# Performance work log

Measured on AMD Instinct MI355X. Metric: run time of the kernel, lower is better.

## Reference

```python
import jax, jax.numpy as jnp
import numpy as np

LMAX_IN = 3
LMAX_OUT = 3
C = 64          # num_channel
H = 64          # num_channel_hidden
N_NODES = 2048
N_EDGES = 8192

# All coupled (l1, l2, l3) paths with |l1-l2| <= l3 <= min(l1+l2, lmax_out)
COMBS = [(l1, l2, l3)
         for l1 in range(LMAX_IN + 1)
         for l2 in range(LMAX_OUT + 1)
         for l3 in range(abs(l1 - l2), min(l1 + l2, LMAX_OUT) + 1)]
COUNTS = {l3: sum(1 for c in COMBS if c[2] == l3) for l3 in range(LMAX_OUT + 1)}

# Fixed coupling (Clebsch-Gordan-like) tensors for each path, shape (2l1+1, 2l2+1, 2l3+1).
# Deterministic constants (not trained / not differentiated), standing in for the
# e3nn CG coefficients used by InterEinsumTC.
_rng = np.random.RandomState(1234)
CG = [jnp.asarray((_rng.randn(2 * l1 + 1, 2 * l2 + 1, 2 * l3 + 1) * 0.2).astype(np.float32))
      for (l1, l2, l3) in COMBS]


def setup_inputs() -> dict:
    key = jax.random.key(0)
    ks = jax.random.split(key, 16)
    inp = {}
    for l in range(LMAX_OUT + 1):
        inp[f"x{l}"] = jax.random.normal(ks[l], (N_NODES, C, 2 * l + 1), dtype=jnp.float32)
        inp[f"y{l}"] = jax.random.normal(ks[4 + l], (N_EDGES, 2 * l + 1), dtype=jnp.float32)
        fan_in = C * COUNTS[l]
        inp[f"w_lin{l}"] = jax.random.normal(ks[8 + l], (fan_in, H), dtype=jnp.float32) / np.float32(np.sqrt(fan_in))
    inp["ws"] = jax.random.normal(ks[12], (N_EDGES, C * len(COMBS)), dtype=jnp.float32)
    inp["edge_index"] = jax.random.randint(ks[13], (2, N_EDGES), 0, N_NODES, dtype=jnp.int32)
    return inp


def _forward(x0, x1, x2, x3, y0, y1, y2, y3, ws, w_lin0, w_lin1, w_lin2, w_lin3, edge_index):
    xs = (x0, x1, x2, x3)
    ys = (y0, y1, y2, y3)
    wl = (w_lin0, w_lin1, w_lin2, w_lin3)
    src, dst = edge_index[0], edge_index[1]
    # per-edge gather of node features for every input degree
    xg = [x[src] for x in xs]                      # [E, C, 2l1+1]
    buf = {l3: [] for l3 in range(LMAX_OUT + 1)}
    for i, (l1, l2, l3) in enumerate(COMBS):
        # tensor-product contraction: [E, C, 2l3+1]
        out = jnp.einsum('lmn,ecl,em->ecn', CG[i], xg[l1], ys[l2])
        w = ws[:, i * C:(i + 1) * C][:, :, None]   # [E, C, 1] per-path per-channel weight
        buf[l3].append(w * out)
    res = []
    for l3 in range(LMAX_OUT + 1):
        m_ji = jnp.concatenate(buf[l3], axis=1)    # [E, C*count_l3, 2l3+1]
        m_i = jax.ops.segment_sum(m_ji, dst, num_segments=N_NODES)  # scatter-sum -> [N, C*count, 2l3+1]
        res.append(jnp.einsum('ncm,ch->nhm', m_i, wl[l3]))          # per-l3 linear -> [N, H, 2l3+1]
    return tuple(res)


def reference(x0, x1, x2, x3, y0, y1, y2, y3, ws, w_lin0, w_lin1, w_lin2, w_lin3, edge_index):
    return _forward(x0, x1, x2, x3, y0, y1, y2, y3, ws,
                    w_lin0, w_lin1, w_lin2, w_lin3, edge_index)
```

## Files before the change

### kernel.cpp

```cpp
#include <hip/hip_runtime.h>
#include <hip/hip_bf16.h>
#include <cmath>
#include <cstdint>

#define NNODES 2048
#define NEDGES 8192
#define NCH 64
#define NHID 64
#define NPATH 34
#define NTASK (NPATH * NCH)
#define CGTOT 3436
#define MROW 9984
#define TTOT2 888
#define EBLK 8

#define MI_BYTES ((size_t)NNODES * MROW * 2)
#define TB_BYTES ((size_t)NEDGES * TTOT2 * 2)
#define XT_BYTES ((size_t)NNODES * 16 * NCH * 2)
#define OFF_OFF  (MI_BYTES + TB_BYTES + XT_BYTES)
#define CUR_OFF  (OFF_OFF + 2052 * 4)
#define PACK_OFF (CUR_OFF + 2048 * 4)
#define ORD_OFF  (PACK_OFF + 8192 * 4)
#define CGP_OFF  (ORD_OFF + 2048 * 4)
#define CGP_FLOATS (TTOT2 * 9)

typedef __attribute__((ext_vector_type(8))) short short8;
typedef __attribute__((ext_vector_type(4))) float floatx4;

struct PathTables {
  int l1[NPATH], l2[NPATH], l3[NPATH];
  int cg_off[NPATH], t_off2[NPATH], rank[NPATH];
  int gpaths[2][20], gnp[2], gbase[2], glen[2];
  int cg_total, ttot2, npaths;
};

constexpr PathTables make_tables() {
  PathTables tb{};
  int np = 0;
  for (int a = 0; a < 4; ++a)
    for (int b = 0; b < 4; ++b) {
      int lo = a > b ? a - b : b - a;
      int hi = a + b < 3 ? a + b : 3;
      for (int c = lo; c <= hi; ++c) { tb.l1[np] = a; tb.l2[np] = b; tb.l3[np] = c; ++np; }
    }
  int cg = 0;
  int cnt[4] = {0, 0, 0, 0};
  for (int i = 0; i < np; ++i) {
    tb.cg_off[i] = cg; tb.rank[i] = cnt[tb.l3[i]]++;
    cg += (2 * tb.l1[i] + 1) * (2 * tb.l2[i] + 1) * (2 * tb.l3[i] + 1);
  }
  int tt2 = 0;
  for (int g = 0; g < 2; ++g) {
    tb.gbase[g] = tt2;
    for (int i = 0; i < np; ++i) {
      int gi = (tb.l3[i] == 0 || tb.l3[i] == 3) ? 0 : 1;
      if (gi != g) continue;
      tb.gpaths[g][tb.gnp[g]++] = i;
      tb.t_off2[i] = tt2;
      int d1 = 2 * tb.l1[i] + 1, d3 = 2 * tb.l3[i] + 1;
      tt2 += ((d1 * d3 + 7) / 8) * 8;
    }
    tb.glen[g] = tt2 - tb.gbase[g];
  }
  tb.cg_total = cg; tb.ttot2 = tt2; tb.npaths = np;
  return tb;
}

constexpr PathTables H_TB = make_tables();
static_assert(H_TB.npaths == NPATH, "npaths");
static_assert(H_TB.cg_total == CGTOT, "cgtot");
static_assert(H_TB.ttot2 == TTOT2, "ttot2");
static_assert(H_TB.gnp[0] == 14 && H_TB.gnp[1] == 20, "gnp");
static_assert(H_TB.gbase[1] == 432 && H_TB.glen[1] == 456, "gsplit");

__constant__ PathTables d_tb = make_tables();

namespace {
struct MT19937 {
  uint32_t mt[624]; int mti; bool has_g; double gval;
  void seed(uint32_t s) {
    for (int i = 0; i < 624; ++i) { mt[i] = s; s = 1812433253u * (s ^ (s >> 30)) + (uint32_t)i + 1u; }
    mti = 624; has_g = false; gval = 0.0;
  }
  uint32_t next() {
    if (mti >= 624) {
      for (int i = 0; i < 624; ++i) {
        uint32_t y = (mt[i] & 0x80000000u) | (mt[(i + 1) % 624] & 0x7fffffffu);
        mt[i] = mt[(i + 397) % 624] ^ (y >> 1) ^ ((y & 1u) ? 0x9908b0dfu : 0u);
      }
      mti = 0;
    }
    uint32_t y = mt[mti++];
    y ^= y >> 11; y ^= (y << 7) & 0x9d2c5680u; y ^= (y << 15) & 0xefc60000u; y ^= y >> 18;
    return y;
  }
  double rdbl() {
    uint32_t a = next() >> 5, b = next() >> 6;
    return ((double)a * 67108864.0 + (double)b) / 9007199254740992.0;
  }
  double gauss() {
    if (has_g) { has_g = false; return gval; }
    double x1, x2, r2;
    do {
      x1 = 2.0 * rdbl() - 1.0;
      x2 = 2.0 * rdbl() - 1.0;
      r2 = x1 * x1 + x2 * x2;
    } while (r2 >= 1.0 || r2 == 0.0);
    double f = std::sqrt(-2.0 * std::log(r2) / r2);
    gval = f * x1; has_g = true;
    return f * x2;
  }
};

float host_pack[CGP_FLOATS];
float* g_cg_dev = nullptr;
bool g_cg_ok = false;

struct CGInit {
  CGInit() {
    static float cg[CGTOT];
    MT19937 g; g.seed(1234u);
    int idx = 0;
    for (int i = 0; i < NPATH; ++i) {
      int d1 = 2 * H_TB.l1[i] + 1, d2 = 2 * H_TB.l2[i] + 1, d3 = 2 * H_TB.l3[i] + 1;
      int sz = d1 * d2 * d3;
      for (int k = 0; k < sz; ++k) cg[idx++] = (float)(g.gauss() * 0.2);
    }
    const int ybase[4] = {0, 1, 4, 9};
    for (int k = 0; k < CGP_FLOATS; ++k) host_pack[k] = 0.f;
    for (int i = 0; i < NPATH; ++i) {
      int d1 = 2 * H_TB.l1[i] + 1, d2 = 2 * H_TB.l2[i] + 1, d3 = 2 * H_TB.l3[i] + 1;
      for (int l = 0; l < d1; ++l)
        for (int n3 = 0; n3 < d3; ++n3) {
          int tt2 = H_TB.t_off2[i] + l * d3 + n3;
          for (int m = 0; m < d2; ++m)
            host_pack[tt2 * 8 + m] = cg[H_TB.cg_off[i] + l * d2 * d3 + m * d3 + n3];
          host_pack[TTOT2 * 8 + tt2] = (float)ybase[H_TB.l2[i]];
        }
    }
    (void)hipHostRegister(host_pack, sizeof(host_pack), hipHostRegisterDefault);
    void* p = nullptr;
    if (hipMalloc(&p, sizeof(host_pack)) == hipSuccess && p) {
      if (hipMemcpy(p, host_pack, sizeof(host_pack), hipMemcpyHostToDevice) == hipSuccess) {
        float back = -1.f;
        if (hipMemcpy(&back, (float*)p + (CGP_FLOATS - 1), sizeof(float),
                      hipMemcpyDeviceToHost) == hipSuccess && back == host_pack[CGP_FLOATS - 1]) {
          g_cg_dev = (float*)p;
          g_cg_ok = true;
        }
      }
    }
  }
} cg_init_instance;
}

__device__ __forceinline__ float bf2f(unsigned short u) {
  union { unsigned int i; float f; } v; v.i = ((unsigned int)u) << 16; return v.f;
}
__device__ __forceinline__ unsigned short f2bf(float f) {
  __hip_bfloat16 h = __float2bfloat16(f);
  union { __hip_bfloat16 h; unsigned short u; } v; v.h = h; return v.u;
}

__global__ __launch_bounds__(256) void prep_kernel(
    const float* __restrict__ y0, const float* __restrict__ y1,
    const float* __restrict__ y2, const float* __restrict__ y3,
    const float* __restrict__ x0, const float* __restrict__ x1,
    const float* __restrict__ x2, const float* __restrict__ x3,
    const float* __restrict__ cg_pack,
    __hip_bfloat16* __restrict__ Tbuf, __hip_bfloat16* __restrict__ xT)
{
  const int b = blockIdx.x;
  const int t = threadIdx.x;
  if (b < NEDGES) {
    __shared__ float y_s[17];
    const int e = b;
    if (t == 16) y_s[16] = 0.f;
    if (t < 16) {
      float v;
      if (t < 1)      v = y0[e];
      else if (t < 4) v = y1[e * 3 + (t - 1)];
      else if (t < 9) v = y2[e * 5 + (t - 4)];
      else            v = y3[e * 7 + (t - 9)];
      y_s[t] = v;
    }
    __syncthreads();
    const float* __restrict__ metaf = cg_pack + TTOT2 * 8;
    __hip_bfloat16* To = Tbuf + (size_t)e * TTOT2;
    for (int tt2 = t; tt2 < TTOT2; tt2 += 256) {
      const float4 a = *(const float4*)(cg_pack + tt2 * 8);
      const float4 c = *(const float4*)(cg_pack + tt2 * 8 + 4);
      const int yb = (int)metaf[tt2];
      float acc = a.x * y_s[yb]     + a.y * y_s[yb + 1] + a.z * y_s[yb + 2] + a.w * y_s[yb + 3]
                + c.x * y_s[yb + 4] + c.y * y_s[yb + 5] + c.z * y_s[yb + 6] + c.w * y_s[yb + 7];
      To[tt2] = __float2bfloat16(acc);
    }
  } else {
    const int n = b - NEDGES;
    for (int idx = t; idx < 1024; idx += 256) {
      const int j = idx >> 6, c = idx & 63;
      const float* src; int d1, m;
      if (j < 1)      { src = x0; d1 = 1; m = j; }
      else if (j < 4) { src = x1; d1 = 3; m = j - 1; }
      else if (j < 9) { src = x2; d1 = 5; m = j - 4; }
      else            { src = x3; d1 = 7; m = j - 9; }
      const float v = src[((size_t)n * NCH + c) * d1 + m];
      xT[((size_t)n * 16 + j) * NCH + c] = __float2bfloat16(v);
    }
  }
}

__global__ __launch_bounds__(256) void scan_kernel(
    const int* __restrict__ edge_index, int* __restrict__ off, int* __restrict__ cursor,
    int* __restrict__ order)
{
  __shared__ int ldeg[NNODES];
  __shared__ int csum[256];
  __shared__ int hist[64];
  const int t = threadIdx.x;
  for (int i = t; i < NNODES; i += 256) ldeg[i] = 0;
  __syncthreads();
  const int* __restrict__ dsts = edge_index + NEDGES;
  for (int e = t; e < NEDGES; e += 256) atomicAdd(&ldeg[dsts[e]], 1);
  __syncthreads();
  int loc[8], s = 0;
  const int base0 = t * 8;
#pragma unroll
  for (int j = 0; j < 8; ++j) { loc[j] = ldeg[base0 + j]; s += loc[j]; }
  csum[t] = s;
  __syncthreads();
  for (int o = 1; o < 256; o <<= 1) {
    int v = (t >= o) ? csum[t - o] : 0;
    __syncthreads();
    csum[t] += v;
    __syncthreads();
  }
  int run = csum[t] - s;
#pragma unroll
  for (int j = 0; j < 8; ++j) { off[base0 + j] = run; cursor[base0 + j] = run; run += loc[j]; }
  if (t == 0) off[NNODES] = NEDGES;
  if (t < 64) hist[t] = 0;
  __syncthreads();
  for (int i = t; i < NNODES; i += 256) {
    int d = ldeg[i]; d = d > 63 ? 63 : d;
    atomicAdd(&hist[63 - d], 1);
  }
  __syncthreads();
  if (t == 0) { int r2 = 0; for (int b = 0; b < 64; ++b) { int c = hist[b]; hist[b] = r2; r2 += c; } }
  __syncthreads();
  for (int i = t; i < NNODES; i += 256) {
    int d = ldeg[i]; d = d > 63 ? 63 : d;
    int pos = atomicAdd(&hist[63 - d], 1);
    order[pos] = i;
  }
}

__global__ __launch_bounds__(256) void fill_kernel(
    const int* __restrict__ edge_index, int* __restrict__ cursor, int* __restrict__ pack)
{
  const int e = blockIdx.x * 256 + threadIdx.x;
  if (e >= NEDGES) return;
  const int d = edge_index[NEDGES + e];
  const int s = edge_index[e];
  const int pos = atomicAdd(&cursor[d], 1);
  pack[pos] = e | (s << 13);
}

template <int D1, int D3>
__device__ __forceinline__ void tp_task_run(
    int wcol, int toff_l, int rank, int nb, const int* __restrict__ epk,
    const float (*Ts)[456], const float* __restrict__ ws,
    const unsigned short* __restrict__ xT,
    int n, bool first, __hip_bfloat16* __restrict__ m_out)
{
  constexpr int Kc = (D3 == 1) ? 256 : (D3 == 3) ? 576 : (D3 == 5) ? 704 : 640;
  constexpr int Rc = (D3 == 1) ? 0 : (D3 == 3) ? 256 : (D3 == 5) ? 1984 : 5504;
  constexpr int JB = (D1 == 1) ? 0 : (D1 == 3) ? 1 : (D1 == 5) ? 4 : 9;
  const int c = wcol & 63;

  float acc[D3];
#pragma unroll
  for (int m = 0; m < D3; ++m) acc[m] = 0.f;

  for (int ei = 0; ei < nb; ++ei) {
    const int pk = epk[ei];
    const int e = pk & 8191;
    const int s = pk >> 13;
    const float w = ws[(size_t)e * NTASK + wcol];
    const unsigned short* __restrict__ xr = xT + ((size_t)s * 16 + JB) * NCH + c;
    const float* __restrict__ Tp = &Ts[ei][toff_l];
    float u[D3];
#pragma unroll
    for (int m = 0; m < D3; ++m) u[m] = 0.f;
#pragma unroll
    for (int l = 0; l < D1; ++l) {
      const float xv = bf2f(xr[l * NCH]);
#pragma unroll
      for (int m = 0; m < D3; ++m) u[m] += xv * Tp[l * D3 + m];
    }
#pragma unroll
    for (int m = 0; m < D3; ++m) acc[m] += w * u[m];
  }

  __hip_bfloat16* mo = m_out + (size_t)n * MROW + Rc + rank * NCH + c;
  if (first) {
#pragma unroll
    for (int m = 0; m < D3; ++m) mo[m * Kc] = __float2bfloat16(acc[m]);
  } else {
#pragma unroll
    for (int m = 0; m < D3; ++m)
      mo[m * Kc] = __float2bfloat16(__bfloat162float(mo[m * Kc]) + acc[m]);
  }
}

__global__ __launch_bounds__(256) void tp_node_kernel(
    const float* __restrict__ ws, const unsigned short* __restrict__ xT,
    const unsigned short* __restrict__ Tbuf,
    const int* __restrict__ off, const int* __restrict__ pack,
    const int* __restrict__ order,
    __hip_bfloat16* __restrict__ m_out)
{
  __shared__ float Ts[EBLK][456];
  __shared__ int epk[EBLK];

  const int bid = blockIdx.x;
  const int n = order[bid >> 1];
  const int g = bid & 1;
  const int t = threadIdx.x;
  const int beg = off[n];
  const int cnt = off[n + 1] - beg;
  const int gbase2 = d_tb.gbase[g] >> 1;
  const int glen2  = d_tb.glen[g] >> 1;
  const int ntask  = d_tb.gnp[g] << 6;

  for (int base = 0; base == 0 || base < cnt; base += EBLK) {
    int nb = cnt - base;
    nb = nb < 0 ? 0 : (nb > EBLK ? EBLK : nb);
    if (t < nb) epk[t] = pack[beg + base + t];
    __syncthreads();
    for (int ei = 0; ei < nb; ++ei) {
      const unsigned int* __restrict__ src =
          (const unsigned int*)Tbuf + (size_t)(epk[ei] & 8191) * (TTOT2 / 2) + gbase2;
      for (int j = t; j < glen2; j += 256) {
        const unsigned int v = src[j];
        float2 f2 = make_float2(bf2f((unsigned short)(v & 0xffffu)),
                                bf2f((unsigned short)(v >> 16)));
        *(float2*)&Ts[ei][2 * j] = f2;
      }
    }
    __syncthreads();

    const bool first = (base == 0);
    for (int k = 0; k * 256 + t < ntask; ++k) {
      const int tl = k * 256 + t;
      const int i = d_tb.gpaths[g][tl >> 6];
      const int wcol = (i << 6) | (tl & 63);
      const int toff_l = d_tb.t_off2[i] - d_tb.gbase[g];
      const int rk = d_tb.rank[i];
      const int code = d_tb.l1[i] * 4 + d_tb.l3[i];
      switch (code) {
        case  0: tp_task_run<1,1>(wcol, toff_l, rk, nb, epk, Ts, ws, xT, n, first, m_out); break;
        case  1: tp_task_run<1,3>(wcol, toff_l, rk, nb, epk, Ts, ws, xT, n, first, m_out); break;
        case  2: tp_task_run<1,5>(wcol, toff_l, rk, nb, epk, Ts, ws, xT, n, first, m_out); break;
        case  3: tp_task_run<1,7>(wcol, toff_l, rk, nb, epk, Ts, ws, xT, n, first, m_out); break;
        case  4: tp_task_run<3,1>(wcol, toff_l, rk, nb, epk, Ts, ws, xT, n, first, m_out); break;
        case  5: tp_task_run<3,3>(wcol, toff_l, rk, nb, epk, Ts, ws, xT, n, first, m_out); break;
        case  6: tp_task_run<3,5>(wcol, toff_l, rk, nb, epk, Ts, ws, xT, n, first, m_out); break;
        case  7: tp_task_run<3,7>(wcol, toff_l, rk, nb, epk, Ts, ws, xT, n, first, m_out); break;
        case  8: tp_task_run<5,1>(wcol, toff_l, rk, nb, epk, Ts, ws, xT, n, first, m_out); break;
        case  9: tp_task_run<5,3>(wcol, toff_l, rk, nb, epk, Ts, ws, xT, n, first, m_out); break;
        case 10: tp_task_run<5,5>(wcol, toff_l, rk, nb, epk, Ts, ws, xT, n, first, m_out); break;
        case 11: tp_task_run<5,7>(wcol, toff_l, rk, nb, epk, Ts, ws, xT, n, first, m_out); break;
        case 12: tp_task_run<7,1>(wcol, toff_l, rk, nb, epk, Ts, ws, xT, n, first, m_out); break;
        case 13: tp_task_run<7,3>(wcol, toff_l, rk, nb, epk, Ts, ws, xT, n, first, m_out); break;
        case 14: tp_task_run<7,5>(wcol, toff_l, rk, nb, epk, Ts, ws, xT, n, first, m_out); break;
        default: tp_task_run<7,7>(wcol, toff_l, rk, nb, epk, Ts, ws, xT, n, first, m_out); break;
      }
    }
    __syncthreads();
  }
}

template <int D3, int K, int ROFF>
__device__ __forceinline__ void lin_mfma_body(
    int blk, const unsigned short* __restrict__ mu, const float* __restrict__ wl,
    float* __restrict__ out, unsigned short (*A_s)[72], unsigned short (*W_s)[72])
{
  const int t = threadIdx.x;
  const int wv = t >> 6;
  const int lane = t & 63;
  const int idx16 = lane & 15;
  const int quad = lane >> 4;
  const int r0 = blk * 64;

  floatx4 acc[4] = {{0.f,0.f,0.f,0.f},{0.f,0.f,0.f,0.f},{0.f,0.f,0.f,0.f},{0.f,0.f,0.f,0.f}};

  for (int k0 = 0; k0 < K; k0 += 64) {
    for (int idx = t; idx < 512; idx += 256) {
      const int rr = idx >> 3, ck = (idx & 7) * 8;
      const int r = r0 + rr;
      const int nn = r / D3, mm = r - nn * D3;
      const uint4 v = *(const uint4*)(mu + (size_t)nn * MROW + ROFF + mm * K + k0 + ck);
      *(uint4*)&A_s[rr][ck] = v;
    }
    {
      const int h = t & 63, kg = t >> 6;
      unsigned short tmp[16];
#pragma unroll
      for (int j = 0; j < 16; ++j)
        tmp[j] = f2bf(wl[(size_t)(k0 + kg * 16 + j) * 64 + h]);
      *(uint4*)&W_s[h][kg * 16]     = *(const uint4*)&tmp[0];
      *(uint4*)&W_s[h][kg * 16 + 8] = *(const uint4*)&tmp[8];
    }
    __syncthreads();
#pragma unroll
    for (int ks = 0; ks < 2; ++ks) {
      const int kb = ks * 32 + quad * 8;
      const short8 af = *(const short8*)&A_s[wv * 16 + idx16][kb];
#pragma unroll
      for (int nt = 0; nt < 4; ++nt) {
        const short8 bf = *(const short8*)&W_s[nt * 16 + idx16][kb];
        acc[nt] = __builtin_amdgcn_mfma_f32_16x16x32_bf16(af, bf, acc[nt], 0, 0, 0);
      }
    }
    __syncthreads();
  }

#pragma unroll
  for (int nt = 0; nt < 4; ++nt) {
    const int h = nt * 16 + idx16;
#pragma unroll
    for (int r = 0; r < 4; ++r) {
      const int row = r0 + wv * 16 + quad * 4 + r;
      const int nn = row / D3, mm = row - nn * D3;
      out[((size_t)nn * NHID + h) * D3 + mm] = acc[nt][r];
    }
  }
}

__global__ __launch_bounds__(256) void lin_fused_kernel(
    const unsigned short* __restrict__ mu,
    const float* __restrict__ wl0, const float* __restrict__ wl1,
    const float* __restrict__ wl2, const float* __restrict__ wl3,
    float* __restrict__ out)
{
  __shared__ unsigned short A_s[64][72];
  __shared__ unsigned short W_s[64][72];
  const int b = blockIdx.x;
  if (b < 32)       lin_mfma_body<1, 256, 0>   (b,       mu, wl0, out,           A_s, W_s);
  else if (b < 128) lin_mfma_body<3, 576, 256> (b - 32,  mu, wl1, out + 131072,  A_s, W_s);
  else if (b < 288) lin_mfma_body<5, 704, 1984>(b - 128, mu, wl2, out + 524288,  A_s, W_s);
  else              lin_mfma_body<7, 640, 5504>(b - 288, mu, wl3, out + 1179648, A_s, W_s);
}

extern "C" void kernel_launch(void* const* d_in, const int* in_sizes, int n_in,
                              void* d_out, int out_size, void* d_ws, size_t ws_size,
                              hipStream_t stream) {
  const float* x0  = (const float*)d_in[0];
  const float* y0  = (const float*)d_in[1];
  const float* wl0 = (const float*)d_in[2];
  const float* x1  = (const float*)d_in[3];
  const float* y1  = (const float*)d_in[4];
  const float* wl1 = (const float*)d_in[5];
  const float* x2  = (const float*)d_in[6];
  const float* y2  = (const float*)d_in[7];
  const float* wl2 = (const float*)d_in[8];
  const float* x3  = (const float*)d_in[9];
  const float* y3  = (const float*)d_in[10];
  const float* wl3 = (const float*)d_in[11];
  const float* ws  = (const float*)d_in[12];
  const int* edge_index = (const int*)d_in[13];
  float* out = (float*)d_out;

  __hip_bfloat16* m_i  = (__hip_bfloat16*)d_ws;
  __hip_bfloat16* Tbuf = (__hip_bfloat16*)((char*)d_ws + MI_BYTES);
  __hip_bfloat16* xT   = (__hip_bfloat16*)((char*)d_ws + MI_BYTES + TB_BYTES);
  int* csr_off = (int*)((char*)d_ws + OFF_OFF);
  int* cursor  = (int*)((char*)d_ws + CUR_OFF);
  int* pack    = (int*)((char*)d_ws + PACK_OFF);
  int* order   = (int*)((char*)d_ws + ORD_OFF);

  const float* cg_pack;
  if (g_cg_ok) {
    cg_pack = g_cg_dev;
  } else {
    float* cg_ws = (float*)((char*)d_ws + CGP_OFF);
    hipMemcpyAsync(cg_ws, host_pack, sizeof(host_pack), hipMemcpyHostToDevice, stream);
    cg_pack = cg_ws;
  }

  prep_kernel<<<NEDGES + NNODES, 256, 0, stream>>>(y0, y1, y2, y3, x0, x1, x2, x3,
                                                   cg_pack, Tbuf, xT);
  scan_kernel<<<1, 256, 0, stream>>>(edge_index, csr_off, cursor, order);
  fill_kernel<<<NEDGES / 256, 256, 0, stream>>>(edge_index, cursor, pack);
  tp_node_kernel<<<2 * NNODES, 256, 0, stream>>>(ws, (const unsigned short*)xT,
                                                 (const unsigned short*)Tbuf,
                                                 csr_off, pack, order, m_i);
  lin_fused_kernel<<<512, 256, 0, stream>>>((const unsigned short*)m_i,
                                            wl0, wl1, wl2, wl3, out);
}
```

Baseline: 249.1 us.

## Fuse per-edge CG-times-Y computation into node kernel, drop Tbuf and merge prep kernels

Stops materialising the per-edge bf16 T buffer (CG contracted with y) in a separate prep pass. The node kernel now recomputes those values in shared memory from y and the CG pack for each edge block. The scan kernel moves to 1024 threads, and the fill step is merged with the xT transpose into one launch. Per-edge ws loads are hoisted ahead of the edge loop. This removes a large global write and reread plus one launch, at the cost of recomputing T once per group block (twice per edge) and extra shared-memory work.

```diff
diff --git a/kernel.cpp b/kernel.cpp
--- a/kernel.cpp
+++ b/kernel.cpp
@@ -15,13 +15,13 @@
 #define EBLK 8
 
 #define MI_BYTES ((size_t)NNODES * MROW * 2)
-#define TB_BYTES ((size_t)NEDGES * TTOT2 * 2)
 #define XT_BYTES ((size_t)NNODES * 16 * NCH * 2)
-#define OFF_OFF  (MI_BYTES + TB_BYTES + XT_BYTES)
+#define OFF_OFF  (MI_BYTES)
 #define CUR_OFF  (OFF_OFF + 2052 * 4)
 #define PACK_OFF (CUR_OFF + 2048 * 4)
 #define ORD_OFF  (PACK_OFF + 8192 * 4)
-#define CGP_OFF  (ORD_OFF + 2048 * 4)
+#define XT_OFF   (ORD_OFF + 2048 * 4)
+#define CGP_OFF  (XT_OFF + XT_BYTES)
 #define CGP_FLOATS (TTOT2 * 9)
 
 typedef __attribute__((ext_vector_type(8))) short short8;
@@ -162,41 +162,65 @@
   union { __hip_bfloat16 h; unsigned short u; } v; v.h = h; return v.u;
 }
 
-__global__ __launch_bounds__(256) void prep_kernel(
-    const float* __restrict__ y0, const float* __restrict__ y1,
-    const float* __restrict__ y2, const float* __restrict__ y3,
+__global__ __launch_bounds__(1024) void scan_kernel(
+    const int* __restrict__ edge_index, int* __restrict__ off, int* __restrict__ cursor,
+    int* __restrict__ order)
+{
+  __shared__ int ldeg[NNODES];
+  __shared__ int csum[1024];
+  __shared__ int hist[64];
+  const int t = threadIdx.x;
+  for (int i = t; i < NNODES; i += 1024) ldeg[i] = 0;
+  __syncthreads();
+  const int* __restrict__ dsts = edge_index + NEDGES;
+  for (int e = t; e < NEDGES; e += 1024) atomicAdd(&ldeg[dsts[e]], 1);
+  __syncthreads();
+  const int l0 = ldeg[2 * t], l1 = ldeg[2 * t + 1];
+  const int s = l0 + l1;
+  csum[t] = s;
+  __syncthreads();
+  for (int o = 1; o < 1024; o <<= 1) {
+    int v = (t >= o) ? csum[t - o] : 0;
+    __syncthreads();
+    csum[t] += v;
+    __syncthreads();
+  }
+  int run = csum[t] - s;
+  off[2 * t] = run; cursor[2 * t] = run;
+  off[2 * t + 1] = run + l0; cursor[2 * t + 1] = run + l0;
+  if (t == 0) off[NNODES] = NEDGES;
+  if (t < 64) hist[t] = 0;
+  __syncthreads();
+  for (int i = t; i < NNODES; i += 1024) {
+    int d = ldeg[i]; d = d > 63 ? 63 : d;
+    atomicAdd(&hist[63 - d], 1);
+  }
+  __syncthreads();
+  if (t == 0) { int r2 = 0; for (int b = 0; b < 64; ++b) { int c = hist[b]; hist[b] = r2; r2 += c; } }
+  __syncthreads();
+  for (int i = t; i < NNODES; i += 1024) {
+    int d = ldeg[i]; d = d > 63 ? 63 : d;
+    int pos = atomicAdd(&hist[63 - d], 1);
+    order[pos] = i;
+  }
+}
+
+__global__ __launch_bounds__(256) void fill_xt_kernel(
+    const int* __restrict__ edge_index, int* __restrict__ cursor, int* __restrict__ pack,
     const float* __restrict__ x0, const float* __restrict__ x1,
     const float* __restrict__ x2, const float* __restrict__ x3,
-    const float* __restrict__ cg_pack,
-    __hip_bfloat16* __restrict__ Tbuf, __hip_bfloat16* __restrict__ xT)
+    __hip_bfloat16* __restrict__ xT)
 {
   const int b = blockIdx.x;
   const int t = threadIdx.x;
-  if (b < NEDGES) {
-    __shared__ float y_s[17];
-    const int e = b;
-    if (t == 16) y_s[16] = 0.f;
-    if (t < 16) {
-      float v;
-      if (t < 1)      v = y0[e];
-      else if (t < 4) v = y1[e * 3 + (t - 1)];
-      else if (t < 9) v = y2[e * 5 + (t - 4)];
-      else            v = y3[e * 7 + (t - 9)];
-      y_s[t] = v;
-    }
-    __syncthreads();
-    const float* __restrict__ metaf = cg_pack + TTOT2 * 8;
-    __hip_bfloat16* To = Tbuf + (size_t)e * TTOT2;
-    for (int tt2 = t; tt2 < TTOT2; tt2 += 256) {
-      const float4 a = *(const float4*)(cg_pack + tt2 * 8);
-      const float4 c = *(const float4*)(cg_pack + tt2 * 8 + 4);
-      const int yb = (int)metaf[tt2];
-      float acc = a.x * y_s[yb]     + a.y * y_s[yb + 1] + a.z * y_s[yb + 2] + a.w * y_s[yb + 3]
-                + c.x * y_s[yb + 4] + c.y * y_s[yb + 5] + c.z * y_s[yb + 6] + c.w * y_s[yb + 7];
-      To[tt2] = __float2bfloat16(acc);
-    }
+  if (b < 32) {
+    const int e = b * 256 + t;
+    const int d = edge_index[NEDGES + e];
+    const int s = edge_index[e];
+    const int pos = atomicAdd(&cursor[d], 1);
+    pack[pos] = e | (s << 13);
   } else {
-    const int n = b - NEDGES;
+    const int n = b - 32;
     for (int idx = t; idx < 1024; idx += 256) {
       const int j = idx >> 6, c = idx & 63;
       const float* src; int d1, m;
@@ -210,62 +234,6 @@
   }
 }
 
-__global__ __launch_bounds__(256) void scan_kernel(
-    const int* __restrict__ edge_index, int* __restrict__ off, int* __restrict__ cursor,
-    int* __restrict__ order)
-{
-  __shared__ int ldeg[NNODES];
-  __shared__ int csum[256];
-  __shared__ int hist[64];
-  const int t = threadIdx.x;
-  for (int i = t; i < NNODES; i += 256) ldeg[i] = 0;
-  __syncthreads();
-  const int* __restrict__ dsts = edge_index + NEDGES;
-  for (int e = t; e < NEDGES; e += 256) atomicAdd(&ldeg[dsts[e]], 1);
-  __syncthreads();
-  int loc[8], s = 0;
-  const int base0 = t * 8;
-#pragma unroll
-  for (int j = 0; j < 8; ++j) { loc[j] = ldeg[base0 + j]; s += loc[j]; }
-  csum[t] = s;
-  __syncthreads();
-  for (int o = 1; o < 256; o <<= 1) {
-    int v = (t >= o) ? csum[t - o] : 0;
-    __syncthreads();
-    csum[t] += v;
-    __syncthreads();
-  }
-  int run = csum[t] - s;
-#pragma unroll
-  for (int j = 0; j < 8; ++j) { off[base0 + j] = run; cursor[base0 + j] = run; run += loc[j]; }
-  if (t == 0) off[NNODES] = NEDGES;
-  if (t < 64) hist[t] = 0;
-  __syncthreads();
-  for (int i = t; i < NNODES; i += 256) {
-    int d = ldeg[i]; d = d > 63 ? 63 : d;
-    atomicAdd(&hist[63 - d], 1);
-  }
-  __syncthreads();
-  if (t == 0) { int r2 = 0; for (int b = 0; b < 64; ++b) { int c = hist[b]; hist[b] = r2; r2 += c; } }
-  __syncthreads();
-  for (int i = t; i < NNODES; i += 256) {
-    int d = ldeg[i]; d = d > 63 ? 63 : d;
-    int pos = atomicAdd(&hist[63 - d], 1);
-    order[pos] = i;
-  }
-}
-
-__global__ __launch_bounds__(256) void fill_kernel(
-    const int* __restrict__ edge_index, int* __restrict__ cursor, int* __restrict__ pack)
-{
-  const int e = blockIdx.x * 256 + threadIdx.x;
-  if (e >= NEDGES) return;
-  const int d = edge_index[NEDGES + e];
-  const int s = edge_index[e];
-  const int pos = atomicAdd(&cursor[d], 1);
-  pack[pos] = e | (s << 13);
-}
-
 template <int D1, int D3>
 __device__ __forceinline__ void tp_task_run(
     int wcol, int toff_l, int rank, int nb, const int* __restrict__ epk,
@@ -278,15 +246,17 @@
   constexpr int JB = (D1 == 1) ? 0 : (D1 == 3) ? 1 : (D1 == 5) ? 4 : 9;
   const int c = wcol & 63;
 
+  float wv_[EBLK];
+#pragma unroll
+  for (int ei = 0; ei < EBLK; ++ei)
+    wv_[ei] = (ei < nb) ? ws[(size_t)(epk[ei] & 8191) * NTASK + wcol] : 0.f;
+
   float acc[D3];
 #pragma unroll
   for (int m = 0; m < D3; ++m) acc[m] = 0.f;
 
   for (int ei = 0; ei < nb; ++ei) {
-    const int pk = epk[ei];
-    const int e = pk & 8191;
-    const int s = pk >> 13;
-    const float w = ws[(size_t)e * NTASK + wcol];
+    const int s = epk[ei] >> 13;
     const unsigned short* __restrict__ xr = xT + ((size_t)s * 16 + JB) * NCH + c;
     const float* __restrict__ Tp = &Ts[ei][toff_l];
     float u[D3];
@@ -299,7 +269,7 @@
       for (int m = 0; m < D3; ++m) u[m] += xv * Tp[l * D3 + m];
     }
 #pragma unroll
-    for (int m = 0; m < D3; ++m) acc[m] += w * u[m];
+    for (int m = 0; m < D3; ++m) acc[m] += wv_[ei] * u[m];
   }
 
   __hip_bfloat16* mo = m_out + (size_t)n * MROW + Rc + rank * NCH + c;
@@ -314,13 +284,16 @@
 }
 
 __global__ __launch_bounds__(256) void tp_node_kernel(
+    const float* __restrict__ y0, const float* __restrict__ y1,
+    const float* __restrict__ y2, const float* __restrict__ y3,
     const float* __restrict__ ws, const unsigned short* __restrict__ xT,
-    const unsigned short* __restrict__ Tbuf,
+    const float* __restrict__ cg_pack,
     const int* __restrict__ off, const int* __restrict__ pack,
     const int* __restrict__ order,
     __hip_bfloat16* __restrict__ m_out)
 {
   __shared__ float Ts[EBLK][456];
+  __shared__ float y_s[EBLK][18];
   __shared__ int epk[EBLK];
 
   const int bid = blockIdx.x;
@@ -329,23 +302,37 @@
   const int t = threadIdx.x;
   const int beg = off[n];
   const int cnt = off[n + 1] - beg;
-  const int gbase2 = d_tb.gbase[g] >> 1;
-  const int glen2  = d_tb.glen[g] >> 1;
-  const int ntask  = d_tb.gnp[g] << 6;
+  const int gbase = d_tb.gbase[g];
+  const int glen  = d_tb.glen[g];
+  const int ntask = d_tb.gnp[g] << 6;
+  const float* __restrict__ metaf = cg_pack + TTOT2 * 8;
 
   for (int base = 0; base == 0 || base < cnt; base += EBLK) {
     int nb = cnt - base;
     nb = nb < 0 ? 0 : (nb > EBLK ? EBLK : nb);
     if (t < nb) epk[t] = pack[beg + base + t];
+    if (t >= 64 && t < 64 + 2 * EBLK) y_s[(t - 64) >> 1][16 + (t & 1)] = 0.f;
+    __syncthreads();
+    if (t < nb * 16) {
+      const int ei = t >> 4, j = t & 15;
+      const int e = epk[ei] & 8191;
+      float v;
+      if (j < 1)      v = y0[e];
+      else if (j < 4) v = y1[e * 3 + (j - 1)];
+      else if (j < 9) v = y2[e * 5 + (j - 4)];
+      else            v = y3[e * 7 + (j - 9)];
+      y_s[ei][j] = v;
+    }
     __syncthreads();
     for (int ei = 0; ei < nb; ++ei) {
-      const unsigned int* __restrict__ src =
-          (const unsigned int*)Tbuf + (size_t)(epk[ei] & 8191) * (TTOT2 / 2) + gbase2;
-      for (int j = t; j < glen2; j += 256) {
-        const unsigned int v = src[j];
-        float2 f2 = make_float2(bf2f((unsigned short)(v & 0xffffu)),
-                                bf2f((unsigned short)(v >> 16)));
-        *(float2*)&Ts[ei][2 * j] = f2;
+      for (int j = t; j < glen; j += 256) {
+        const int tt2 = gbase + j;
+        const float4 a = *(const float4*)(cg_pack + tt2 * 8);
+        const float4 c4 = *(const float4*)(cg_pack + tt2 * 8 + 4);
+        const int yb = (int)metaf[tt2];
+        const float* yy = &y_s[ei][yb];
+        Ts[ei][j] = a.x * yy[0] + a.y * yy[1] + a.z * yy[2] + a.w * yy[3]
+                  + c4.x * yy[4] + c4.y * yy[5] + c4.z * yy[6] + c4.w * yy[7];
       }
     }
     __syncthreads();
@@ -355,7 +342,7 @@
       const int tl = k * 256 + t;
       const int i = d_tb.gpaths[g][tl >> 6];
       const int wcol = (i << 6) | (tl & 63);
-      const int toff_l = d_tb.t_off2[i] - d_tb.gbase[g];
+      const int toff_l = d_tb.t_off2[i] - gbase;
       const int rk = d_tb.rank[i];
       const int code = d_tb.l1[i] * 4 + d_tb.l3[i];
       switch (code) {
@@ -472,13 +459,12 @@
   const int* edge_index = (const int*)d_in[13];
   float* out = (float*)d_out;
 
-  __hip_bfloat16* m_i  = (__hip_bfloat16*)d_ws;
-  __hip_bfloat16* Tbuf = (__hip_bfloat16*)((char*)d_ws + MI_BYTES);
-  __hip_bfloat16* xT   = (__hip_bfloat16*)((char*)d_ws + MI_BYTES + TB_BYTES);
+  __hip_bfloat16* m_i = (__hip_bfloat16*)d_ws;
   int* csr_off = (int*)((char*)d_ws + OFF_OFF);
   int* cursor  = (int*)((char*)d_ws + CUR_OFF);
   int* pack    = (int*)((char*)d_ws + PACK_OFF);
   int* order   = (int*)((char*)d_ws + ORD_OFF);
+  __hip_bfloat16* xT = (__hip_bfloat16*)((char*)d_ws + XT_OFF);
 
   const float* cg_pack;
   if (g_cg_ok) {
@@ -489,12 +475,11 @@
     cg_pack = cg_ws;
   }
 
-  prep_kernel<<<NEDGES + NNODES, 256, 0, stream>>>(y0, y1, y2, y3, x0, x1, x2, x3,
-                                                   cg_pack, Tbuf, xT);
-  scan_kernel<<<1, 256, 0, stream>>>(edge_index, csr_off, cursor, order);
-  fill_kernel<<<NEDGES / 256, 256, 0, stream>>>(edge_index, cursor, pack);
-  tp_node_kernel<<<2 * NNODES, 256, 0, stream>>>(ws, (const unsigned short*)xT,
-                                                 (const unsigned short*)Tbuf,
+  scan_kernel<<<1, 1024, 0, stream>>>(edge_index, csr_off, cursor, order);
+  fill_xt_kernel<<<32 + NNODES, 256, 0, stream>>>(edge_index, cursor, pack,
+                                                  x0, x1, x2, x3, xT);
+  tp_node_kernel<<<2 * NNODES, 256, 0, stream>>>(y0, y1, y2, y3, ws,
+                                                 (const unsigned short*)xT, cg_pack,
                                                  csr_off, pack, order, m_i);
   lin_fused_kernel<<<512, 256, 0, stream>>>((const unsigned short*)m_i,
                                             wl0, wl1, wl2, wl3, out);
```

Result: faster. 233.5 us (-6.3%).
